# Kernel tuning notes

Measured on AMD Instinct MI355X. Metric: run time of the kernel, lower is better.

The kernel has to match this reference:

```python
import jax, jax.numpy as jnp
import numpy as np

EPS = 1e-7
STRIDE = 1
PAD = 3


def _mantissa_map(v):
    # (|v|+eps) * 2^(-floor(log2(|v|+eps))) - 1  -> mantissa-1 in [0,1)
    a = jnp.abs(v) + EPS
    base = a * jnp.exp2(-jnp.floor(jnp.log2(a))) - 1.0
    # piecewise: >=0.5 -> (1+base)/2, else 1+base  (values in [0.75, 1.5))
    return jnp.where(base >= 0.5, (1.0 + base) * 0.5, 1.0 + base)


def _unfold(x, kH, kW, stride, pad, Ho, Wo):
    # im2col matching torch.nn.Unfold ordering (kernel position index = i*kW + j)
    xp = jnp.pad(x, ((0, 0), (0, 0), (pad, pad), (pad, pad)))
    cols = [xp[:, :, i:i + stride * Ho:stride, j:j + stride * Wo:stride]
            for i in range(kH) for j in range(kW)]
    return jnp.stack(cols, axis=-1)  # (B, C, Ho, Wo, kH*kW)


def setup_inputs() -> dict:
    key = jax.random.key(0)
    k1, k2 = jax.random.split(key)
    x = jax.random.normal(k1, (4, 192, 56, 56), dtype=jnp.float32)
    weight = jax.random.normal(k2, (192, 1, 7, 7), dtype=jnp.float32) * 0.1
    return {"x": x, "weight": weight}


def reference(x, weight):
    B, C, H, W = x.shape
    _, _, kH, kW = weight.shape
    Ho = (H + 2 * PAD - kH) // STRIDE + 1
    Wo = (W + 2 * PAD - kW) // STRIDE + 1
    KK = kH * kW

    # mantissa factors
    m2 = _mantissa_map(weight).reshape(C, KK)[None, :, None, None, :]  # (1,C,1,1,KK)
    m1 = _unfold(_mantissa_map(x), kH, kW, STRIDE, PAD, Ho, Wo)        # (B,C,Ho,Wo,KK)
    # zeros come only from unfold's zero padding; map them to 1 (then 0 after -1)
    m1 = jnp.where(m1 == 0.0, 1.0, m1) - 1.0
    m2 = m2 - 1.0

    factor = (m1 + m2 + 1.0) / ((m1 + 1.0) * (m2 + 1.0))
    factor = jnp.where(jnp.isfinite(factor), factor, 1.0)

    q_x = _unfold(x, kH, kW, STRIDE, PAD, Ho, Wo)          # (B,C,Ho,Wo,KK)
    w = weight.reshape(C, KK)[None, :, None, None, :]       # (1,C,1,1,KK)
    q_y = jnp.sum(factor * (q_x * w), axis=-1)              # (B,C,Ho,Wo)
    return q_y.astype(jnp.float32)
```

## Files before the change

### kernel.cpp

```cpp
#include <hip/hip_runtime.h>

typedef float v2f __attribute__((ext_vector_type(2)));
typedef float v4f __attribute__((ext_vector_type(4)));

#define EPS 1e-7f
#define SPW 66

__device__ __forceinline__ float mant_map(float v) {
    float a = fabsf(v) + EPS;
    unsigned int bi = __float_as_uint(a);
    float m = __uint_as_float((bi & 0x007FFFFFu) | 0x3F800000u);
    return (m >= 1.5f) ? 0.5f * m : m;
}

__global__ __launch_bounds__(128, 3) void wconv_kernel(const float* __restrict__ x,
                                                       const float* __restrict__ w,
                                                       float* __restrict__ out) {
    __shared__ v2f sp[34][SPW];
    __shared__ v2f swt[49];

    const int lx = threadIdx.x;
    const int ty = threadIdx.y;
    const int tid = ty * 32 + lx;
    const int c = blockIdx.x;
    const int b = blockIdx.y;
    const int tz = blockIdx.z;

    const int y0 = 28 * tz;
    const int g0 = (tz == 0) ? 0 : 25;
    const int l0 = (tz == 0) ? 3 : 0;
    const int z0 = (tz == 0) ? 0 : 31;

    const long plane = (long)(b * 192 + c) * 3136;
    const float* xp = x + plane;

    if (tid < 49) {
        float wv = w[c * 49 + tid];
        float M2 = mant_map(wv);
        float B = wv / M2;
        swt[tid] = (v2f){B, B * (M2 - 1.0f)};
    }

    for (int t = tid; t < 3 * SPW; t += 128)
        ((v2f*)sp)[z0 * SPW + t] = (v2f){0.f, 0.f};
    for (int t = tid; t < 310; t += 128) {
        int r = t / 10, k = t % 10;
        int col = (k < 3) ? k : 56 + k;
        sp[l0 + r][col] = (v2f){0.f, 0.f};
    }

    for (int t = tid; t < 434; t += 128) {
        int r = t / 14, q4 = t % 14;
        v4f u4 = *(const v4f*)(xp + (g0 + r) * 56 + q4 * 4);
        v2f* dst = &sp[l0 + r][3 + q4 * 4];
        dst[0] = (v2f){u4.x, u4.x * __builtin_amdgcn_rcpf(mant_map(u4.x))};
        dst[1] = (v2f){u4.y, u4.y * __builtin_amdgcn_rcpf(mant_map(u4.y))};
        dst[2] = (v2f){u4.z, u4.z * __builtin_amdgcn_rcpf(mant_map(u4.z))};
        dst[3] = (v2f){u4.w, u4.w * __builtin_amdgcn_rcpf(mant_map(u4.w))};
    }
    __syncthreads();

    if (lx < 28) {
        v2f W[49];
        #pragma unroll
        for (int t = 0; t < 49; ++t) W[t] = swt[t];

        const int x0 = lx * 2;
        const int rb = ty * 7;

        v2f a0[7], a1[7];
        #pragma unroll
        for (int r = 0; r < 7; ++r) { a0[r] = (v2f){0.f, 0.f}; a1[r] = (v2f){0.f, 0.f}; }

        #pragma unroll
        for (int ir = 0; ir < 13; ++ir) {
            const v4f* q = (const v4f*)&sp[rb + ir][x0];
            v4f q0 = q[0], q1 = q[1], q2 = q[2], q3 = q[3];
            v2f p[8] = {{q0.x, q0.y}, {q0.z, q0.w}, {q1.x, q1.y}, {q1.z, q1.w},
                        {q2.x, q2.y}, {q2.z, q2.w}, {q3.x, q3.y}, {q3.z, q3.w}};
            #pragma unroll
            for (int ry = 0; ry < 7; ++ry) {
                const int i = ir - ry;
                if (i >= 0 && i <= 6) {
                    #pragma unroll
                    for (int j = 0; j < 7; ++j) {
                        v2f wc = W[i * 7 + j];
                        a0[ry] += p[j] * wc;
                        a1[ry] += p[j + 1] * wc;
                    }
                }
            }
        }

        #pragma unroll
        for (int ry = 0; ry < 7; ++ry) {
            float2 o = make_float2(a0[ry].x + a0[ry].y, a1[ry].x + a1[ry].y);
            *(float2*)&out[plane + (y0 + rb + ry) * 56 + x0] = o;
        }
    }
}

extern "C" void kernel_launch(void* const* d_in, const int* in_sizes, int n_in,
                              void* d_out, int out_size, void* d_ws, size_t ws_size,
                              hipStream_t stream) {
    const float* x = (const float*)d_in[0];
    const float* w = (const float*)d_in[1];
    float* out = (float*)d_out;

    hipLaunchKernelGGL(wconv_kernel, dim3(192, 4, 2), dim3(32, 4), 0, stream, x, w, out);
}
```

Before: 69.55 us.

## Process whole plane per block and split weights into scalar and vector registers

Each block now covers a full 56x56 channel plane with 256 threads instead of two half-plane blocks, which removes the duplicated 6-row halo load and its mantissa preprocessing. Global loads are issued up front in an unrolled batch before staging into shared memory. The packed-v2f FMAs are split into scalar FMAs: the B weight goes through readfirstlane so it can sit in SGPRs, and the C weight stays in VGPRs behind an asm barrier. This lowers VGPR pressure, but it gives up packed FMA issue, halves the grid to 768 blocks, and raises shared memory use per block.

```diff
diff --git a/kernel.cpp b/kernel.cpp
--- a/kernel.cpp
+++ b/kernel.cpp
@@ -13,10 +13,10 @@
     return (m >= 1.5f) ? 0.5f * m : m;
 }
 
-__global__ __launch_bounds__(128, 3) void wconv_kernel(const float* __restrict__ x,
+__global__ __launch_bounds__(256, 3) void wconv_kernel(const float* __restrict__ x,
                                                        const float* __restrict__ w,
                                                        float* __restrict__ out) {
-    __shared__ v2f sp[34][SPW];
+    __shared__ v2f sp[62][SPW];
     __shared__ v2f swt[49];
 
     const int lx = threadIdx.x;
@@ -24,12 +24,6 @@
     const int tid = ty * 32 + lx;
     const int c = blockIdx.x;
     const int b = blockIdx.y;
-    const int tz = blockIdx.z;
-
-    const int y0 = 28 * tz;
-    const int g0 = (tz == 0) ? 0 : 25;
-    const int l0 = (tz == 0) ? 3 : 0;
-    const int z0 = (tz == 0) ? 0 : 31;
 
     const long plane = (long)(b * 192 + c) * 3136;
     const float* xp = x + plane;
@@ -41,52 +35,73 @@
         swt[tid] = (v2f){B, B * (M2 - 1.0f)};
     }
 
-    for (int t = tid; t < 3 * SPW; t += 128)
-        ((v2f*)sp)[z0 * SPW + t] = (v2f){0.f, 0.f};
-    for (int t = tid; t < 310; t += 128) {
+    for (int t = tid; t < 3 * SPW; t += 256) {
+        ((v2f*)sp)[t] = (v2f){0.f, 0.f};
+        ((v2f*)sp)[59 * SPW + t] = (v2f){0.f, 0.f};
+    }
+    for (int t = tid; t < 560; t += 256) {
         int r = t / 10, k = t % 10;
         int col = (k < 3) ? k : 56 + k;
-        sp[l0 + r][col] = (v2f){0.f, 0.f};
+        sp[3 + r][col] = (v2f){0.f, 0.f};
     }
 
-    for (int t = tid; t < 434; t += 128) {
-        int r = t / 14, q4 = t % 14;
-        v4f u4 = *(const v4f*)(xp + (g0 + r) * 56 + q4 * 4);
-        v2f* dst = &sp[l0 + r][3 + q4 * 4];
-        dst[0] = (v2f){u4.x, u4.x * __builtin_amdgcn_rcpf(mant_map(u4.x))};
-        dst[1] = (v2f){u4.y, u4.y * __builtin_amdgcn_rcpf(mant_map(u4.y))};
-        dst[2] = (v2f){u4.z, u4.z * __builtin_amdgcn_rcpf(mant_map(u4.z))};
-        dst[3] = (v2f){u4.w, u4.w * __builtin_amdgcn_rcpf(mant_map(u4.w))};
+    {
+        const int t0 = tid, t1 = tid + 256, t2 = tid + 512;
+        v4f u0 = *(const v4f*)(xp + (t0 / 14) * 56 + (t0 % 14) * 4);
+        v4f u1 = *(const v4f*)(xp + (t1 / 14) * 56 + (t1 % 14) * 4);
+        v4f u2 = *(const v4f*)(xp + (t2 / 14) * 56 + (t2 % 14) * 4);
+        v4f u3;
+        if (tid < 16) u3 = *(const v4f*)(xp + ((tid + 768) / 14) * 56 + ((tid + 768) % 14) * 4);
+
+        auto stage = [&](int t, v4f u4) {
+            v2f* dst = &sp[3 + t / 14][3 + (t % 14) * 4];
+            dst[0] = (v2f){u4.x, u4.x * __builtin_amdgcn_rcpf(mant_map(u4.x))};
+            dst[1] = (v2f){u4.y, u4.y * __builtin_amdgcn_rcpf(mant_map(u4.y))};
+            dst[2] = (v2f){u4.z, u4.z * __builtin_amdgcn_rcpf(mant_map(u4.z))};
+            dst[3] = (v2f){u4.w, u4.w * __builtin_amdgcn_rcpf(mant_map(u4.w))};
+        };
+        stage(t0, u0);
+        stage(t1, u1);
+        stage(t2, u2);
+        if (tid < 16) stage(tid + 768, u3);
     }
     __syncthreads();
 
+    float sB[49], vC[49];
+    #pragma unroll
+    for (int t = 0; t < 49; ++t) {
+        v2f wc = swt[t];
+        sB[t] = __uint_as_float(__builtin_amdgcn_readfirstlane(__float_as_uint(wc.x)));
+        vC[t] = wc.y;
+    }
+    #pragma unroll
+    for (int t = 0; t < 49; ++t) asm volatile("" : "+v"(vC[t]));
+
     if (lx < 28) {
-        v2f W[49];
-        #pragma unroll
-        for (int t = 0; t < 49; ++t) W[t] = swt[t];
-
         const int x0 = lx * 2;
         const int rb = ty * 7;
 
-        v2f a0[7], a1[7];
+        float a0x[7], a0y[7], a1x[7], a1y[7];
         #pragma unroll
-        for (int r = 0; r < 7; ++r) { a0[r] = (v2f){0.f, 0.f}; a1[r] = (v2f){0.f, 0.f}; }
+        for (int r = 0; r < 7; ++r) { a0x[r] = a0y[r] = a1x[r] = a1y[r] = 0.f; }
 
         #pragma unroll
         for (int ir = 0; ir < 13; ++ir) {
             const v4f* q = (const v4f*)&sp[rb + ir][x0];
             v4f q0 = q[0], q1 = q[1], q2 = q[2], q3 = q[3];
-            v2f p[8] = {{q0.x, q0.y}, {q0.z, q0.w}, {q1.x, q1.y}, {q1.z, q1.w},
-                        {q2.x, q2.y}, {q2.z, q2.w}, {q3.x, q3.y}, {q3.z, q3.w}};
+            float pu[8] = {q0.x, q0.z, q1.x, q1.z, q2.x, q2.z, q3.x, q3.z};
+            float pv[8] = {q0.y, q0.w, q1.y, q1.w, q2.y, q2.w, q3.y, q3.w};
             #pragma unroll
             for (int ry = 0; ry < 7; ++ry) {
                 const int i = ir - ry;
                 if (i >= 0 && i <= 6) {
                     #pragma unroll
                     for (int j = 0; j < 7; ++j) {
-                        v2f wc = W[i * 7 + j];
-                        a0[ry] += p[j] * wc;
-                        a1[ry] += p[j + 1] * wc;
+                        const int t = i * 7 + j;
+                        a0x[ry] = fmaf(pu[j],     sB[t], a0x[ry]);
+                        a0y[ry] = fmaf(pv[j],     vC[t], a0y[ry]);
+                        a1x[ry] = fmaf(pu[j + 1], sB[t], a1x[ry]);
+                        a1y[ry] = fmaf(pv[j + 1], vC[t], a1y[ry]);
                     }
                 }
             }
@@ -94,8 +109,8 @@
 
         #pragma unroll
         for (int ry = 0; ry < 7; ++ry) {
-            float2 o = make_float2(a0[ry].x + a0[ry].y, a1[ry].x + a1[ry].y);
-            *(float2*)&out[plane + (y0 + rb + ry) * 56 + x0] = o;
+            float2 o = make_float2(a0x[ry] + a0y[ry], a1x[ry] + a1y[ry]);
+            *(float2*)&out[plane + (rb + ry) * 56 + x0] = o;
         }
     }
 }
@@ -107,5 +122,5 @@
     const float* w = (const float*)d_in[1];
     float* out = (float*)d_out;
 
-    hipLaunchKernelGGL(wconv_kernel, dim3(192, 4, 2), dim3(32, 4), 0, stream, x, w, out);
+    hipLaunchKernelGGL(wconv_kernel, dim3(192, 4), dim3(32, 8), 0, stream, x, w, out);
 }
```

Result: slower. 94.85 us (+36.4%).

## Shrink row tile to 8 rows per block with rolling two-row register window

Applied to the files above, without the earlier changes.

Each block now covers 8 output rows instead of 28, and the grid grows from 2 to 7 tiles per plane. Each thread computes 2 output rows and streams input rows through two ping-ponged register buffers. Weights are read from shared memory on the fly instead of being held in 49 registers, and staging uses 16-byte LDS writes. Occupancy rises (launch bounds raised to 4 blocks per CU) and register pressure falls, at the cost of more halo re-reads (14 staged rows for 8 output rows) and repeated mantissa preprocessing of those halo rows.

```diff
diff --git a/kernel.cpp b/kernel.cpp
--- a/kernel.cpp
+++ b/kernel.cpp
@@ -13,10 +13,10 @@
     return (m >= 1.5f) ? 0.5f * m : m;
 }
 
-__global__ __launch_bounds__(128, 3) void wconv_kernel(const float* __restrict__ x,
+__global__ __launch_bounds__(128, 4) void wconv_kernel(const float* __restrict__ x,
                                                        const float* __restrict__ w,
                                                        float* __restrict__ out) {
-    __shared__ v2f sp[34][SPW];
+    __shared__ v2f sp[14][SPW];
     __shared__ v2f swt[49];
 
     const int lx = threadIdx.x;
@@ -24,12 +24,7 @@
     const int tid = ty * 32 + lx;
     const int c = blockIdx.x;
     const int b = blockIdx.y;
-    const int tz = blockIdx.z;
-
-    const int y0 = 28 * tz;
-    const int g0 = (tz == 0) ? 0 : 25;
-    const int l0 = (tz == 0) ? 3 : 0;
-    const int z0 = (tz == 0) ? 0 : 31;
+    const int y0 = blockIdx.z * 8;
 
     const long plane = (long)(b * 192 + c) * 3136;
     const float* xp = x + plane;
@@ -41,61 +36,80 @@
         swt[tid] = (v2f){B, B * (M2 - 1.0f)};
     }
 
-    for (int t = tid; t < 3 * SPW; t += 128)
-        ((v2f*)sp)[z0 * SPW + t] = (v2f){0.f, 0.f};
-    for (int t = tid; t < 310; t += 128) {
-        int r = t / 10, k = t % 10;
+    if (tid < 84) {
+        int r = tid / 6, k = tid % 6;
         int col = (k < 3) ? k : 56 + k;
-        sp[l0 + r][col] = (v2f){0.f, 0.f};
+        sp[r][col] = (v2f){0.f, 0.f};
     }
 
-    for (int t = tid; t < 434; t += 128) {
-        int r = t / 14, q4 = t % 14;
-        v4f u4 = *(const v4f*)(xp + (g0 + r) * 56 + q4 * 4);
-        v2f* dst = &sp[l0 + r][3 + q4 * 4];
-        dst[0] = (v2f){u4.x, u4.x * __builtin_amdgcn_rcpf(mant_map(u4.x))};
-        dst[1] = (v2f){u4.y, u4.y * __builtin_amdgcn_rcpf(mant_map(u4.y))};
-        dst[2] = (v2f){u4.z, u4.z * __builtin_amdgcn_rcpf(mant_map(u4.z))};
-        dst[3] = (v2f){u4.w, u4.w * __builtin_amdgcn_rcpf(mant_map(u4.w))};
+    {
+        const int t0 = tid, t1 = tid + 128;
+        const int r0 = t0 / 14, q0 = t0 % 14;
+        const int r1 = t1 / 14, q1 = t1 % 14;
+        const int g0 = y0 - 3 + r0, g1 = y0 - 3 + r1;
+
+        v4f u0 = (v4f){0.f, 0.f, 0.f, 0.f}, u1 = u0;
+        if (g0 >= 0 && g0 < 56) u0 = *(const v4f*)(xp + g0 * 56 + q0 * 4);
+        if (t1 < 196 && g1 >= 0 && g1 < 56) u1 = *(const v4f*)(xp + g1 * 56 + q1 * 4);
+
+        auto stage = [&](int r, int q, v4f u4) {
+            v4f* dst = (v4f*)&sp[r][3 + q * 4];
+            dst[0] = (v4f){u4.x, u4.x * __builtin_amdgcn_rcpf(mant_map(u4.x)),
+                           u4.y, u4.y * __builtin_amdgcn_rcpf(mant_map(u4.y))};
+            dst[1] = (v4f){u4.z, u4.z * __builtin_amdgcn_rcpf(mant_map(u4.z)),
+                           u4.w, u4.w * __builtin_amdgcn_rcpf(mant_map(u4.w))};
+        };
+        stage(r0, q0, u0);
+        if (t1 < 196) stage(r1, q1, u1);
     }
     __syncthreads();
 
-    if (lx < 28) {
-        v2f W[49];
-        #pragma unroll
-        for (int t = 0; t < 49; ++t) W[t] = swt[t];
+    {
+        const int x0 = ((lx < 28) ? lx : 27) * 2;
+        const int rb = ty * 2;
 
-        const int x0 = lx * 2;
-        const int rb = ty * 7;
-
-        v2f a0[7], a1[7];
-        #pragma unroll
-        for (int r = 0; r < 7; ++r) { a0[r] = (v2f){0.f, 0.f}; a1[r] = (v2f){0.f, 0.f}; }
-
-        #pragma unroll
-        for (int ir = 0; ir < 13; ++ir) {
-            const v4f* q = (const v4f*)&sp[rb + ir][x0];
-            v4f q0 = q[0], q1 = q[1], q2 = q[2], q3 = q[3];
-            v2f p[8] = {{q0.x, q0.y}, {q0.z, q0.w}, {q1.x, q1.y}, {q1.z, q1.w},
-                        {q2.x, q2.y}, {q2.z, q2.w}, {q3.x, q3.y}, {q3.z, q3.w}};
-            #pragma unroll
-            for (int ry = 0; ry < 7; ++ry) {
-                const int i = ir - ry;
-                if (i >= 0 && i <= 6) {
-                    #pragma unroll
-                    for (int j = 0; j < 7; ++j) {
-                        v2f wc = W[i * 7 + j];
-                        a0[ry] += p[j] * wc;
-                        a1[ry] += p[j + 1] * wc;
-                    }
-                }
-            }
+#define LOADROW(P, R)                                                   \
+        {                                                               \
+            const v4f* s_ = (const v4f*)&sp[(R)][x0];                   \
+            v4f t0_ = s_[0], t1_ = s_[1], t2_ = s_[2], t3_ = s_[3];     \
+            P[0] = (v2f){t0_.x, t0_.y}; P[1] = (v2f){t0_.z, t0_.w};     \
+            P[2] = (v2f){t1_.x, t1_.y}; P[3] = (v2f){t1_.z, t1_.w};     \
+            P[4] = (v2f){t2_.x, t2_.y}; P[5] = (v2f){t2_.z, t2_.w};     \
+            P[6] = (v2f){t3_.x, t3_.y}; P[7] = (v2f){t3_.z, t3_.w};     \
         }
 
-        #pragma unroll
-        for (int ry = 0; ry < 7; ++ry) {
-            float2 o = make_float2(a0[ry].x + a0[ry].y, a1[ry].x + a1[ry].y);
-            *(float2*)&out[plane + (y0 + rb + ry) * 56 + x0] = o;
+        v2f RA[8], RB[8];
+        LOADROW(RA, rb);
+        LOADROW(RB, rb + 1);
+
+        v2f a00 = {0.f, 0.f}, a01 = {0.f, 0.f};
+        v2f a10 = {0.f, 0.f}, a11 = {0.f, 0.f};
+
+#define STEP(i, P, Q)                                                   \
+        {                                                               \
+            _Pragma("unroll")                                           \
+            for (int j = 0; j < 7; ++j) {                               \
+                v2f wc = swt[(i) * 7 + j];                              \
+                a00 += P[j] * wc;  a01 += P[j + 1] * wc;                \
+                a10 += Q[j] * wc;  a11 += Q[j + 1] * wc;                \
+            }                                                           \
+        }
+
+        STEP(0, RA, RB) LOADROW(RA, rb + 2)
+        STEP(1, RB, RA) LOADROW(RB, rb + 3)
+        STEP(2, RA, RB) LOADROW(RA, rb + 4)
+        STEP(3, RB, RA) LOADROW(RB, rb + 5)
+        STEP(4, RA, RB) LOADROW(RA, rb + 6)
+        STEP(5, RB, RA) LOADROW(RB, rb + 7)
+        STEP(6, RA, RB)
+#undef STEP
+#undef LOADROW
+
+        if (lx < 28) {
+            float2 o0 = make_float2(a00.x + a00.y, a01.x + a01.y);
+            float2 o1 = make_float2(a10.x + a10.y, a11.x + a11.y);
+            *(float2*)&out[plane + (y0 + rb)     * 56 + x0] = o0;
+            *(float2*)&out[plane + (y0 + rb + 1) * 56 + x0] = o1;
         }
     }
 }
@@ -107,5 +121,5 @@
     const float* w = (const float*)d_in[1];
     float* out = (float*)d_out;
 
-    hipLaunchKernelGGL(wconv_kernel, dim3(192, 4, 2), dim3(32, 4), 0, stream, x, w, out);
+    hipLaunchKernelGGL(wconv_kernel, dim3(192, 4, 7), dim3(32, 4), 0, stream, x, w, out);
 }
```

New measurement: 71.31 us. 1.03x slower.
